# Optimization experiments

Measured on AMD Instinct MI355X. Metric: run time of the kernel, lower is better.

The kernel has to match this reference:

```python
import jax, jax.numpy as jnp
import numpy as np

B, N, D, H = 2, 2048, 1024, 16
DH = D // H
DF = 4 * D
SCALE = D ** (-0.5)  # standard_scale=False -> dim**-0.5
EPS = 1e-5


def _ln(x, w, b):
    mu = jnp.mean(x, axis=-1, keepdims=True)
    var = jnp.mean(jnp.square(x - mu), axis=-1, keepdims=True)
    return (x - mu) * jax.lax.rsqrt(var + EPS) * w + b


def setup_inputs() -> dict:
    key = jax.random.key(0)
    ks = jax.random.split(key, 12)
    s = lambda fan_in: (1.0 / np.sqrt(fan_in))
    return {
        "x": jax.random.normal(ks[0], (B, N, D), jnp.float32),
        "gamma": jax.random.uniform(ks[1], (B, H), jnp.float32),
        "dist_matrix": jax.random.uniform(ks[2], (N, N), jnp.float32),
        "ln1_w": jnp.ones((D,), jnp.float32),
        "ln1_b": jnp.zeros((D,), jnp.float32),
        "qkv_w": jax.random.normal(ks[3], (D, 3 * D), jnp.float32) * s(D),
        "qkv_b": jnp.zeros((3 * D,), jnp.float32),
        "proj_w": jax.random.normal(ks[4], (D, D), jnp.float32) * s(D),
        "proj_b": jnp.zeros((D,), jnp.float32),
        "ln2_w": jnp.ones((D,), jnp.float32),
        "ln2_b": jnp.zeros((D,), jnp.float32),
        "mlp_w1": jax.random.normal(ks[5], (D, DF), jnp.float32) * s(D),
        "mlp_b1": jnp.zeros((DF,), jnp.float32),
        "mlp_w2": jax.random.normal(ks[6], (DF, D), jnp.float32) * s(DF),
        "mlp_b2": jnp.zeros((D,), jnp.float32),
    }


def reference(x, gamma, dist_matrix, ln1_w, ln1_b, qkv_w, qkv_b, proj_w, proj_b,
              ln2_w, ln2_b, mlp_w1, mlp_b1, mlp_w2, mlp_b2):
    # --- ZoomAttention on norm1(x) ---
    h = _ln(x, ln1_w, ln1_b)                                   # [B,N,D]
    qkv = h @ qkv_w + qkv_b                                    # [B,N,3D]
    qkv = qkv.reshape(B, N, 3, H, DH).transpose(2, 0, 3, 1, 4)  # [3,B,H,N,DH]
    q, k, v = qkv[0], qkv[1], qkv[2]
    scores = jnp.einsum("bhnd,bhmd->bhnm", q, k) * SCALE       # [B,H,N,N]
    scores = scores - gamma[:, :, None, None] * dist_matrix[None, None]
    attn = jax.nn.softmax(scores, axis=-1)
    out = jnp.einsum("bhnm,bhmd->bhnd", attn, v)               # [B,H,N,DH]
    out = out.transpose(0, 2, 1, 3).reshape(B, N, D)
    x = x + (out @ proj_w + proj_b)
    # --- MLP (exact GELU, torch default) ---
    h2 = _ln(x, ln2_w, ln2_b)
    h2 = jax.nn.gelu(h2 @ mlp_w1 + mlp_b1, approximate=False) @ mlp_w2 + mlp_b2
    return x + h2
```

## Files before the change

### kernel.cpp

```cpp
#include <hip/hip_runtime.h>
#include <hip/hip_bf16.h>


#define SCALE_ 0.03125f
#define EPS_   1e-5f
#define LOG2E_ 1.4426950408889634f
#define SC2_   (SCALE_ * LOG2E_)

typedef unsigned short u16;
typedef __attribute__((ext_vector_type(8))) short short8;
typedef __attribute__((ext_vector_type(4))) float f32x4;
typedef __attribute__((ext_vector_type(4))) unsigned short u16x4;

__device__ inline float b2f(u16 u){ unsigned x = ((unsigned)u) << 16; float f; __builtin_memcpy(&f, &x, 4); return f; }
__device__ inline u16 f2b(float f){ __hip_bfloat16 h = __float2bfloat16(f); u16 u; __builtin_memcpy(&u, &h, 2); return u; }

__device__ inline void glds16(const u16* g, u16* l) {
    __builtin_amdgcn_global_load_lds(
        (const __attribute__((address_space(1))) void*)g,
        (__attribute__((address_space(3))) void*)l, 16, 0, 0);
}

__global__ __launch_bounds__(256) void transpose_cast(const float* __restrict__ src,
                                                      u16* __restrict__ dst, int K, int N) {
    __shared__ float t[32][33];
    int nb = blockIdx.x * 32, kb = blockIdx.y * 32;
    int tx = threadIdx.x & 31, ty = threadIdx.x >> 5;
    for (int i = 0; i < 4; i++) {
        int r = ty + i * 8;
        t[r][tx] = src[(size_t)(kb + r) * N + nb + tx];
    }
    __syncthreads();
    for (int i = 0; i < 4; i++) {
        int r = ty + i * 8;
        dst[(size_t)(nb + r) * K + kb + tx] = f2b(t[tx][r]);
    }
}

__global__ __launch_bounds__(256) void cast_scale_bf16(const float* __restrict__ src,
                                                       u16* __restrict__ dst, int n4, float scale) {
    int i = blockIdx.x * 256 + threadIdx.x;
    if (i < n4) {
        float4 v = ((const float4*)src)[i];
        u16x4 o;
        o[0] = f2b(v.x * scale); o[1] = f2b(v.y * scale);
        o[2] = f2b(v.z * scale); o[3] = f2b(v.w * scale);
        ((u16x4*)dst)[i] = o;
    }
}

__global__ __launch_bounds__(256) void ln_bf16(const float* __restrict__ x,
                                               const float* __restrict__ w,
                                               const float* __restrict__ b,
                                               u16* __restrict__ out) {
    int row = blockIdx.x, t = threadIdx.x;
    float4 v = ((const float4*)(x + (size_t)row * 1024))[t];
    float s1 = v.x + v.y + v.z + v.w;
    float s2 = v.x * v.x + v.y * v.y + v.z * v.z + v.w * v.w;
    for (int o = 32; o > 0; o >>= 1) { s1 += __shfl_xor(s1, o); s2 += __shfl_xor(s2, o); }
    __shared__ float a1[4], a2[4];
    if ((t & 63) == 0) { a1[t >> 6] = s1; a2[t >> 6] = s2; }
    __syncthreads();
    s1 = a1[0] + a1[1] + a1[2] + a1[3];
    s2 = a2[0] + a2[1] + a2[2] + a2[3];
    float mu = s1 * (1.0f / 1024.0f);
    float var = s2 * (1.0f / 1024.0f) - mu * mu;
    float rs = rsqrtf(var + EPS_);
    float4 wv = ((const float4*)w)[t];
    float4 bv = ((const float4*)b)[t];
    u16x4 o;
    o[0] = f2b((v.x - mu) * rs * wv.x + bv.x);
    o[1] = f2b((v.y - mu) * rs * wv.y + bv.y);
    o[2] = f2b((v.z - mu) * rs * wv.z + bv.z);
    o[3] = f2b((v.w - mu) * rs * wv.w + bv.w);
    ((u16x4*)(out + (size_t)row * 1024))[t] = o;
}

template <int MODE, int BN>
__global__ __launch_bounds__(256) void gemm_bf16(
    const u16* __restrict__ A, const u16* __restrict__ Bt,
    const float* __restrict__ bias, int M, int N, int K,
    const float* __restrict__ res, float* __restrict__ outf, u16* __restrict__ outb,
    u16* __restrict__ qp, u16* __restrict__ kp, u16* __restrict__ vtp) {
    constexpr int NN = BN / 32;
    __shared__ u16 As[128 * 64];
    __shared__ u16 Bs[BN * 64];
    int br = blockIdx.y * 128, bc = blockIdx.x * BN;
    int tid = threadIdx.x;
    int w = tid >> 6, lane = tid & 63, g = lane >> 4, ln = lane & 15;
    int wr = (w >> 1) * 64, wc = (w & 1) * (BN / 2);
    f32x4 acc[4][NN] = {};
    int sgcol = (((lane & 7) ^ (lane >> 3)) << 3);
    int arow = w * 32 + (lane >> 3);
    int brow = w * (BN / 4) + (lane >> 3);
    const u16* Ap = A + (size_t)(br + arow) * K + sgcol;
    const u16* Bp = Bt + (size_t)(bc + brow) * K + sgcol;
    u16* lA = &As[(w * 32) * 64];
    u16* lB = &Bs[(w * (BN / 4)) * 64];
    size_t rstep = (size_t)8 * K;
    for (int kt = 0; kt < K; kt += 64) {
        __syncthreads();
        #pragma unroll
        for (int i = 0; i < 4; i++) glds16(Ap + kt + i * rstep, lA + i * 512);
        #pragma unroll
        for (int i = 0; i < BN / 32; i++) glds16(Bp + kt + i * rstep, lB + i * 512);
        __syncthreads();
        #pragma unroll
        for (int kk = 0; kk < 2; kk++) {
            int so = (((kk << 2) + g) ^ (ln & 7)) << 3;
            short8 af[4], bfr[NN];
            #pragma unroll
            for (int m = 0; m < 4; m++)  af[m]  = *(const short8*)&As[(wr + m * 16 + ln) * 64 + so];
            #pragma unroll
            for (int n = 0; n < NN; n++) bfr[n] = *(const short8*)&Bs[(wc + n * 16 + ln) * 64 + so];
            #pragma unroll
            for (int m = 0; m < 4; m++)
                #pragma unroll
                for (int n = 0; n < NN; n++)
                    acc[m][n] = __builtin_amdgcn_mfma_f32_16x16x32_bf16(af[m], bfr[n], acc[m][n], 0, 0, 0);
        }
    }
    #pragma unroll
    for (int m = 0; m < 4; m++) {
        int row0 = br + wr + m * 16 + g * 4;
        #pragma unroll
        for (int n = 0; n < NN; n++) {
            int col = bc + wc + n * 16 + ln;
            float bv = bias[col];
            if constexpr (MODE == 0) {
                int which = col >> 10, cc = col & 1023, hh = cc >> 6, dh = cc & 63;
                int bb = row0 >> 11, nn0 = row0 & 2047;
                size_t bh = (size_t)(bb * 16 + hh);
                if (which == 0) {
                    for (int r = 0; r < 4; r++)
                        qp[((bh * 2048 + nn0 + r) << 6) + dh] = f2b((acc[m][n][r] + bv) * SC2_);
                } else if (which == 1) {
                    for (int r = 0; r < 4; r++)
                        kp[((bh * 2048 + nn0 + r) << 6) + dh] = f2b(acc[m][n][r] + bv);
                } else {
                    u16x4 o;
                    for (int r = 0; r < 4; r++) o[r] = f2b(acc[m][n][r] + bv);
                    *(u16x4*)&vtp[((bh * 64 + dh) << 11) + nn0] = o;
                }
            } else if constexpr (MODE == 1) {
                for (int r = 0; r < 4; r++) {
                    size_t idx = (size_t)(row0 + r) * 1024 + col;
                    outf[idx] = res[idx] + acc[m][n][r] + bv;
                }
            } else if constexpr (MODE == 2) {
                for (int r = 0; r < 4; r++) {
                    float v = acc[m][n][r] + bv;
                    float gl = 0.5f * v * (1.0f + erff(v * 0.7071067811865476f));
                    outb[(size_t)(row0 + r) * 4096 + col] = f2b(gl);
                }
            } else {
                for (int r = 0; r < 4; r++) {
                    size_t idx = (size_t)(row0 + r) * 1024 + col;
                    outf[idx] = outf[idx] + acc[m][n][r] + bv;
                }
            }
        }
    }
}

__global__ __launch_bounds__(256) void attn_fwd(
    const u16* __restrict__ qg, const u16* __restrict__ kg, const u16* __restrict__ vtg,
    const u16* __restrict__ distb, const float* __restrict__ gamma, u16* __restrict__ ao) {
    __shared__ u16 Ks[2][64 * 64];
    __shared__ u16 Vs[2][64 * 64];
    __shared__ u16 Ps[4][16 * 64];
    int qt = blockIdx.x, bh = blockIdx.y;
    int b = bh >> 4, h = bh & 15;
    int tid = threadIdx.x, w = tid >> 6, lane = tid & 63, g = lane >> 4, ln = lane & 15;
    float gam = gamma[bh];
    int qglob = qt * 64 + w * 16 + ln;
    const u16* qrow = qg + ((size_t)bh * 2048 + qglob) * 64;
    short8 qf0 = *(const short8*)(qrow + g * 8);
    short8 qf1 = *(const short8*)(qrow + 32 + g * 8);
    const u16* dbase = distb + (size_t)qglob * 2048 + g * 4;
    float m2 = -3.0e38f, lsum = 0.0f;
    f32x4 acco[4] = {};
    int srow = tid >> 2, sc = (tid & 3) * 2;
    int ss0 = ((sc ^ (srow & 7)) << 3), ss1 = (((sc + 1) ^ (srow & 7)) << 3);
    const u16* kgp = kg + ((size_t)bh * 2048 + srow) * 64 + sc * 8;
    const u16* vgp = vtg + ((size_t)bh * 64 + srow) * 2048 + sc * 8;
    {
        short8 a0 = *(const short8*)(kgp);
        short8 a1 = *(const short8*)(kgp + 8);
        short8 c0 = *(const short8*)(vgp);
        short8 c1 = *(const short8*)(vgp + 8);
        *(short8*)&Ks[0][srow * 64 + ss0] = a0;
        *(short8*)&Ks[0][srow * 64 + ss1] = a1;
        *(short8*)&Vs[0][srow * 64 + ss0] = c0;
        *(short8*)&Vs[0][srow * 64 + ss1] = c1;
    }
    u16x4 dcv[4];
    #pragma unroll
    for (int nb = 0; nb < 4; nb++) dcv[nb] = *(const u16x4*)(dbase + nb * 16);
    __syncthreads();
    int cur = 0;
    int so0 = (g ^ (ln & 7)) << 3, so1 = ((4 + g) ^ (ln & 7)) << 3;
    for (int kt = 0; kt < 32; kt++) {
        short8 kr0, kr1, vr0, vr1;
        u16x4 dnx[4];
        if (kt < 31) {
            kr0 = *(const short8*)(kgp + (kt + 1) * 4096);
            kr1 = *(const short8*)(kgp + (kt + 1) * 4096 + 8);
            vr0 = *(const short8*)(vgp + (kt + 1) * 64);
            vr1 = *(const short8*)(vgp + (kt + 1) * 64 + 8);
            #pragma unroll
            for (int nb = 0; nb < 4; nb++)
                dnx[nb] = *(const u16x4*)(dbase + (kt + 1) * 64 + nb * 16);
        }
        f32x4 sa[4] = {};
        __builtin_amdgcn_s_setprio(1);
        #pragma unroll
        for (int nb = 0; nb < 4; nb++) {
            short8 kf0 = *(const short8*)&Ks[cur][(nb * 16 + ln) * 64 + so0];
            short8 kf1 = *(const short8*)&Ks[cur][(nb * 16 + ln) * 64 + so1];
            sa[nb] = __builtin_amdgcn_mfma_f32_16x16x32_bf16(kf0, qf0, sa[nb], 0, 0, 0);
            sa[nb] = __builtin_amdgcn_mfma_f32_16x16x32_bf16(kf1, qf1, sa[nb], 0, 0, 0);
        }
        __builtin_amdgcn_s_setprio(0);
        float sv[4][4], pm = -3.0e38f;
        #pragma unroll
        for (int nb = 0; nb < 4; nb++)
            #pragma unroll
            for (int r = 0; r < 4; r++) {
                float s = sa[nb][r] - gam * b2f(dcv[nb][r]);
                sv[nb][r] = s;
                pm = fmaxf(pm, s);
            }
        pm = fmaxf(pm, __shfl_xor(pm, 16));
        pm = fmaxf(pm, __shfl_xor(pm, 32));
        if (!__all(pm - m2 <= 8.0f)) {
            float nm = fmaxf(m2, pm);
            float al = __builtin_exp2f(m2 - nm);
            m2 = nm;
            lsum *= al;
            #pragma unroll
            for (int db = 0; db < 4; db++) acco[db] *= al;
        }
        float ps = 0.0f;
        #pragma unroll
        for (int nb = 0; nb < 4; nb++) {
            u16x4 pw;
            #pragma unroll
            for (int r = 0; r < 4; r++) {
                float p = __builtin_exp2f(sv[nb][r] - m2);
                ps += p;
                pw[r] = f2b(p);
            }
            int off = nb * 16 + g * 4;
            *(u16x4*)&Ps[w][ln * 64 + (((off >> 3) ^ (ln & 7)) << 3) + (off & 7)] = pw;
        }
        ps += __shfl_xor(ps, 16);
        ps += __shfl_xor(ps, 32);
        lsum += ps;
        short8 pf0 = *(const short8*)&Ps[w][ln * 64 + so0];
        short8 pf1 = *(const short8*)&Ps[w][ln * 64 + so1];
        __builtin_amdgcn_s_setprio(1);
        #pragma unroll
        for (int db = 0; db < 4; db++) {
            short8 vf0 = *(const short8*)&Vs[cur][(db * 16 + ln) * 64 + so0];
            short8 vf1 = *(const short8*)&Vs[cur][(db * 16 + ln) * 64 + so1];
            acco[db] = __builtin_amdgcn_mfma_f32_16x16x32_bf16(vf0, pf0, acco[db], 0, 0, 0);
            acco[db] = __builtin_amdgcn_mfma_f32_16x16x32_bf16(vf1, pf1, acco[db], 0, 0, 0);
        }
        __builtin_amdgcn_s_setprio(0);
        if (kt < 31) {
            int nx = cur ^ 1;
            *(short8*)&Ks[nx][srow * 64 + ss0] = kr0;
            *(short8*)&Ks[nx][srow * 64 + ss1] = kr1;
            *(short8*)&Vs[nx][srow * 64 + ss0] = vr0;
            *(short8*)&Vs[nx][srow * 64 + ss1] = vr1;
            #pragma unroll
            for (int nb = 0; nb < 4; nb++) dcv[nb] = dnx[nb];
            __syncthreads();
            cur = nx;
        }
    }
    float inv = 1.0f / lsum;
    u16* aop = ao + (size_t)(b * 2048 + qglob) * 1024 + h * 64 + g * 4;
    #pragma unroll
    for (int db = 0; db < 4; db++) {
        u16x4 o;
        #pragma unroll
        for (int r = 0; r < 4; r++) o[r] = f2b(acco[db][r] * inv);
        *(u16x4*)(aop + db * 16) = o;
    }
}

extern "C" void kernel_launch(void* const* d_in, const int* in_sizes, int n_in,
                              void* d_out, int out_size, void* d_ws, size_t ws_size,
                              hipStream_t stream) {
    const float* x     = (const float*)d_in[0];
    const float* gamma = (const float*)d_in[1];
    const float* dist  = (const float*)d_in[2];
    const float* ln1w  = (const float*)d_in[3];
    const float* ln1b  = (const float*)d_in[4];
    const float* qkvw  = (const float*)d_in[5];
    const float* qkvb  = (const float*)d_in[6];
    const float* projw = (const float*)d_in[7];
    const float* projb = (const float*)d_in[8];
    const float* ln2w  = (const float*)d_in[9];
    const float* ln2b  = (const float*)d_in[10];
    const float* w1    = (const float*)d_in[11];
    const float* b1    = (const float*)d_in[12];
    const float* w2    = (const float*)d_in[13];
    const float* b2    = (const float*)d_in[14];
    float* out = (float*)d_out;
    char* ws = (char*)d_ws;
    u16* wqkvT  = (u16*)(ws + 0);
    u16* wprojT = (u16*)(ws + 6291456);
    u16* w1T    = (u16*)(ws + 8388608);
    u16* w2T    = (u16*)(ws + 16777216);
    u16* distb  = (u16*)(ws + 25165824);
    u16* hb     = (u16*)(ws + 33554432);
    u16* qb     = (u16*)(ws + 41943040);
    u16* kb     = (u16*)(ws + 50331648);
    u16* vtb    = (u16*)(ws + 58720256);
    u16* aob    = (u16*)(ws + 67108864);
    u16* gb     = hb;
    u16* h2b    = aob;

    dim3 blk(256);
    transpose_cast<<<dim3(3072 / 32, 1024 / 32), blk, 0, stream>>>(qkvw, wqkvT, 1024, 3072);
    transpose_cast<<<dim3(1024 / 32, 1024 / 32), blk, 0, stream>>>(projw, wprojT, 1024, 1024);
    transpose_cast<<<dim3(4096 / 32, 1024 / 32), blk, 0, stream>>>(w1, w1T, 1024, 4096);
    transpose_cast<<<dim3(1024 / 32, 4096 / 32), blk, 0, stream>>>(w2, w2T, 4096, 1024);
    cast_scale_bf16<<<4096, blk, 0, stream>>>(dist, distb, 2048 * 2048 / 4, LOG2E_);
    ln_bf16<<<4096, blk, 0, stream>>>(x, ln1w, ln1b, hb);
    gemm_bf16<0, 128><<<dim3(24, 32), blk, 0, stream>>>(hb, wqkvT, qkvb, 4096, 3072, 1024,
                                                        nullptr, nullptr, nullptr, qb, kb, vtb);
    attn_fwd<<<dim3(32, 32), blk, 0, stream>>>(qb, kb, vtb, distb, gamma, aob);
    gemm_bf16<1, 64><<<dim3(16, 32), blk, 0, stream>>>(aob, wprojT, projb, 4096, 1024, 1024,
                                                       x, out, nullptr, nullptr, nullptr, nullptr);
    ln_bf16<<<4096, blk, 0, stream>>>(out, ln2w, ln2b, h2b);
    gemm_bf16<2, 128><<<dim3(32, 32), blk, 0, stream>>>(h2b, w1T, b1, 4096, 4096, 1024,
                                                        nullptr, nullptr, gb, nullptr, nullptr, nullptr);
    gemm_bf16<3, 64><<<dim3(16, 32), blk, 0, stream>>>(gb, w2T, b2, 4096, 1024, 4096,
                                                       nullptr, out, nullptr, nullptr, nullptr, nullptr);
}
```

Measured before the change: 297.8 us.

## Add 256x256 pipelined GEMM, read fp32 dist directly, compute row sums via MFMA

```diff
diff --git a/kernel.cpp b/kernel.cpp
--- a/kernel.cpp
+++ b/kernel.cpp
@@ -34,18 +34,6 @@
     for (int i = 0; i < 4; i++) {
         int r = ty + i * 8;
         dst[(size_t)(nb + r) * K + kb + tx] = f2b(t[tx][r]);
-    }
-}
-
-__global__ __launch_bounds__(256) void cast_scale_bf16(const float* __restrict__ src,
-                                                       u16* __restrict__ dst, int n4, float scale) {
-    int i = blockIdx.x * 256 + threadIdx.x;
-    if (i < n4) {
-        float4 v = ((const float4*)src)[i];
-        u16x4 o;
-        o[0] = f2b(v.x * scale); o[1] = f2b(v.y * scale);
-        o[2] = f2b(v.z * scale); o[3] = f2b(v.w * scale);
-        ((u16x4*)dst)[i] = o;
     }
 }
 
@@ -76,12 +64,128 @@
     ((u16x4*)(out + (size_t)row * 1024))[t] = o;
 }
 
+template <int MODE>
+__global__ __launch_bounds__(512) void gemm256_8ph(
+    const u16* __restrict__ A, const u16* __restrict__ Bt,
+    const float* __restrict__ bias, int K,
+    u16* __restrict__ outb,
+    u16* __restrict__ qp, u16* __restrict__ kp, u16* __restrict__ vtp) {
+    __shared__ u16 LS[4][2][256 * 32];
+    int tid = threadIdx.x;
+    int w = tid >> 6, lane = tid & 63, g = lane >> 4, ln = lane & 15;
+    int wr = w >> 2, wc = w & 3;
+    int gx = gridDim.x;
+    int nwg = gx * gridDim.y;
+    int lin = blockIdx.y * gx + blockIdx.x;
+    int swz = (lin & 7) * (nwg >> 3) + (lin >> 3);
+    int bx = swz % gx, by = swz / gx;
+    int br = by * 256, bc = bx * 256;
+    int jx = (((lane & 3) ^ ((lane >> 3) & 3)) << 3);
+    const u16* Ast = A + (size_t)(br + w * 32 + (lane >> 2)) * K + jx;
+    const u16* Bst = Bt + (size_t)(bc + w * 32 + (lane >> 2)) * K + jx;
+    size_t r16 = (size_t)16 * K;
+    const int ldsW = (w * 32) * 32;
+    f32x4 acc[8][4] = {};
+    int NT = K >> 5;
+    int slotr = ((g ^ ((ln >> 1) & 3)) << 3);
+    for (int kt = 0; kt < 3; ++kt) {
+        glds16(Ast + (size_t)kt * 32, &LS[kt][0][ldsW]);
+        glds16(Ast + (size_t)kt * 32 + r16, &LS[kt][0][ldsW + 512]);
+        glds16(Bst + (size_t)kt * 32, &LS[kt][1][ldsW]);
+        glds16(Bst + (size_t)kt * 32 + r16, &LS[kt][1][ldsW + 512]);
+    }
+    asm volatile("s_waitcnt vmcnt(8)" ::: "memory");
+    __builtin_amdgcn_s_barrier();
+    short8 aa[4], bb[4];
+    for (int kt = 0; kt < NT; ++kt) {
+        const u16* bufA = &LS[kt & 3][0][0];
+        const u16* bufB = &LS[kt & 3][1][0];
+        int s3 = kt + 3;
+        #pragma unroll
+        for (int m = 0; m < 4; ++m)
+            aa[m] = *(const short8*)&bufA[(wr * 128 + m * 16 + ln) * 32 + slotr];
+        #pragma unroll
+        for (int n = 0; n < 4; ++n)
+            bb[n] = *(const short8*)&bufB[(wc * 64 + n * 16 + ln) * 32 + slotr];
+        if (s3 < NT) {
+            u16* d = &LS[s3 & 3][0][ldsW];
+            glds16(Ast + (size_t)s3 * 32, d);
+            glds16(Ast + (size_t)s3 * 32 + r16, d + 512);
+        }
+        __builtin_amdgcn_s_barrier();
+        asm volatile("s_waitcnt lgkmcnt(0)" ::: "memory");
+        __builtin_amdgcn_sched_barrier(0);
+        __builtin_amdgcn_s_setprio(1);
+        #pragma unroll
+        for (int m = 0; m < 4; ++m)
+            #pragma unroll
+            for (int n = 0; n < 4; ++n)
+                acc[m][n] = __builtin_amdgcn_mfma_f32_16x16x32_bf16(aa[m], bb[n], acc[m][n], 0, 0, 0);
+        __builtin_amdgcn_s_setprio(0);
+        __builtin_amdgcn_sched_barrier(0);
+        __builtin_amdgcn_s_barrier();
+        #pragma unroll
+        for (int m = 0; m < 4; ++m)
+            aa[m] = *(const short8*)&bufA[(wr * 128 + 64 + m * 16 + ln) * 32 + slotr];
+        if (s3 < NT) {
+            u16* d = &LS[s3 & 3][1][ldsW];
+            glds16(Bst + (size_t)s3 * 32, d);
+            glds16(Bst + (size_t)s3 * 32 + r16, d + 512);
+        }
+        if (kt + 3 < NT)      asm volatile("s_waitcnt vmcnt(8)" ::: "memory");
+        else if (kt + 2 < NT) asm volatile("s_waitcnt vmcnt(4)" ::: "memory");
+        else if (kt + 1 < NT) asm volatile("s_waitcnt vmcnt(0)" ::: "memory");
+        __builtin_amdgcn_s_barrier();
+        asm volatile("s_waitcnt lgkmcnt(0)" ::: "memory");
+        __builtin_amdgcn_sched_barrier(0);
+        __builtin_amdgcn_s_setprio(1);
+        #pragma unroll
+        for (int m = 0; m < 4; ++m)
+            #pragma unroll
+            for (int n = 0; n < 4; ++n)
+                acc[4 + m][n] = __builtin_amdgcn_mfma_f32_16x16x32_bf16(aa[m], bb[n], acc[4 + m][n], 0, 0, 0);
+        __builtin_amdgcn_s_setprio(0);
+        __builtin_amdgcn_sched_barrier(0);
+        __builtin_amdgcn_s_barrier();
+    }
+    #pragma unroll
+    for (int m = 0; m < 8; ++m) {
+        int row0 = br + wr * 128 + m * 16 + g * 4;
+        #pragma unroll
+        for (int n = 0; n < 4; ++n) {
+            int col = bc + wc * 64 + n * 16 + ln;
+            float bv = bias[col];
+            if constexpr (MODE == 0) {
+                int which = col >> 10, cc = col & 1023, hh = cc >> 6, dh = cc & 63;
+                int bb2 = row0 >> 11, nn0 = row0 & 2047;
+                size_t bh = (size_t)(bb2 * 16 + hh);
+                if (which == 0) {
+                    for (int r = 0; r < 4; r++)
+                        qp[((bh * 2048 + nn0 + r) << 6) + dh] = f2b((acc[m][n][r] + bv) * SC2_);
+                } else if (which == 1) {
+                    for (int r = 0; r < 4; r++)
+                        kp[((bh * 2048 + nn0 + r) << 6) + dh] = f2b(acc[m][n][r] + bv);
+                } else {
+                    u16x4 o;
+                    for (int r = 0; r < 4; r++) o[r] = f2b(acc[m][n][r] + bv);
+                    *(u16x4*)&vtp[((bh * 64 + dh) << 11) + nn0] = o;
+                }
+            } else {
+                for (int r = 0; r < 4; r++) {
+                    float v = acc[m][n][r] + bv;
+                    float gl = 0.5f * v * (1.0f + erff(v * 0.7071067811865476f));
+                    outb[(size_t)(row0 + r) * 4096 + col] = f2b(gl);
+                }
+            }
+        }
+    }
+}
+
 template <int MODE, int BN>
 __global__ __launch_bounds__(256) void gemm_bf16(
     const u16* __restrict__ A, const u16* __restrict__ Bt,
     const float* __restrict__ bias, int M, int N, int K,
-    const float* __restrict__ res, float* __restrict__ outf, u16* __restrict__ outb,
-    u16* __restrict__ qp, u16* __restrict__ kp, u16* __restrict__ vtp) {
+    const float* __restrict__ res, float* __restrict__ outf) {
     constexpr int NN = BN / 32;
     __shared__ u16 As[128 * 64];
     __shared__ u16 Bs[BN * 64];
@@ -127,31 +231,10 @@
         for (int n = 0; n < NN; n++) {
             int col = bc + wc + n * 16 + ln;
             float bv = bias[col];
-            if constexpr (MODE == 0) {
-                int which = col >> 10, cc = col & 1023, hh = cc >> 6, dh = cc & 63;
-                int bb = row0 >> 11, nn0 = row0 & 2047;
-                size_t bh = (size_t)(bb * 16 + hh);
-                if (which == 0) {
-                    for (int r = 0; r < 4; r++)
-                        qp[((bh * 2048 + nn0 + r) << 6) + dh] = f2b((acc[m][n][r] + bv) * SC2_);
-                } else if (which == 1) {
-                    for (int r = 0; r < 4; r++)
-                        kp[((bh * 2048 + nn0 + r) << 6) + dh] = f2b(acc[m][n][r] + bv);
-                } else {
-                    u16x4 o;
-                    for (int r = 0; r < 4; r++) o[r] = f2b(acc[m][n][r] + bv);
-                    *(u16x4*)&vtp[((bh * 64 + dh) << 11) + nn0] = o;
-                }
-            } else if constexpr (MODE == 1) {
+            if constexpr (MODE == 1) {
                 for (int r = 0; r < 4; r++) {
                     size_t idx = (size_t)(row0 + r) * 1024 + col;
                     outf[idx] = res[idx] + acc[m][n][r] + bv;
-                }
-            } else if constexpr (MODE == 2) {
-                for (int r = 0; r < 4; r++) {
-                    float v = acc[m][n][r] + bv;
-                    float gl = 0.5f * v * (1.0f + erff(v * 0.7071067811865476f));
-                    outb[(size_t)(row0 + r) * 4096 + col] = f2b(gl);
                 }
             } else {
                 for (int r = 0; r < 4; r++) {
@@ -165,21 +248,25 @@
 
 __global__ __launch_bounds__(256) void attn_fwd(
     const u16* __restrict__ qg, const u16* __restrict__ kg, const u16* __restrict__ vtg,
-    const u16* __restrict__ distb, const float* __restrict__ gamma, u16* __restrict__ ao) {
+    const float* __restrict__ dist, const float* __restrict__ gamma, u16* __restrict__ ao) {
     __shared__ u16 Ks[2][64 * 64];
     __shared__ u16 Vs[2][64 * 64];
     __shared__ u16 Ps[4][16 * 64];
     int qt = blockIdx.x, bh = blockIdx.y;
     int b = bh >> 4, h = bh & 15;
     int tid = threadIdx.x, w = tid >> 6, lane = tid & 63, g = lane >> 4, ln = lane & 15;
-    float gam = gamma[bh];
+    float gam2 = gamma[bh] * LOG2E_;
     int qglob = qt * 64 + w * 16 + ln;
     const u16* qrow = qg + ((size_t)bh * 2048 + qglob) * 64;
     short8 qf0 = *(const short8*)(qrow + g * 8);
     short8 qf1 = *(const short8*)(qrow + 32 + g * 8);
-    const u16* dbase = distb + (size_t)qglob * 2048 + g * 4;
-    float m2 = -3.0e38f, lsum = 0.0f;
+    const float* dbase = dist + (size_t)qglob * 2048 + g * 4;
+    float m2 = -3.0e38f;
     f32x4 acco[4] = {};
+    f32x4 accl = {};
+    short8 ones;
+    #pragma unroll
+    for (int i = 0; i < 8; ++i) ones[i] = (short)0x3F80;
     int srow = tid >> 2, sc = (tid & 3) * 2;
     int ss0 = ((sc ^ (srow & 7)) << 3), ss1 = (((sc + 1) ^ (srow & 7)) << 3);
     const u16* kgp = kg + ((size_t)bh * 2048 + srow) * 64 + sc * 8;
@@ -194,15 +281,15 @@
         *(short8*)&Vs[0][srow * 64 + ss0] = c0;
         *(short8*)&Vs[0][srow * 64 + ss1] = c1;
     }
-    u16x4 dcv[4];
+    float4 dcv[4];
     #pragma unroll
-    for (int nb = 0; nb < 4; nb++) dcv[nb] = *(const u16x4*)(dbase + nb * 16);
+    for (int nb = 0; nb < 4; nb++) dcv[nb] = *(const float4*)(dbase + nb * 16);
     __syncthreads();
     int cur = 0;
     int so0 = (g ^ (ln & 7)) << 3, so1 = ((4 + g) ^ (ln & 7)) << 3;
     for (int kt = 0; kt < 32; kt++) {
         short8 kr0, kr1, vr0, vr1;
-        u16x4 dnx[4];
+        float4 dnx[4];
         if (kt < 31) {
             kr0 = *(const short8*)(kgp + (kt + 1) * 4096);
             kr1 = *(const short8*)(kgp + (kt + 1) * 4096 + 8);
@@ -210,7 +297,7 @@
             vr1 = *(const short8*)(vgp + (kt + 1) * 64 + 8);
             #pragma unroll
             for (int nb = 0; nb < 4; nb++)
-                dnx[nb] = *(const u16x4*)(dbase + (kt + 1) * 64 + nb * 16);
+                dnx[nb] = *(const float4*)(dbase + (kt + 1) * 64 + nb * 16);
         }
         f32x4 sa[4] = {};
         __builtin_amdgcn_s_setprio(1);
@@ -224,39 +311,33 @@
         __builtin_amdgcn_s_setprio(0);
         float sv[4][4], pm = -3.0e38f;
         #pragma unroll
-        for (int nb = 0; nb < 4; nb++)
-            #pragma unroll
-            for (int r = 0; r < 4; r++) {
-                float s = sa[nb][r] - gam * b2f(dcv[nb][r]);
-                sv[nb][r] = s;
-                pm = fmaxf(pm, s);
-            }
+        for (int nb = 0; nb < 4; nb++) {
+            float4 dv = dcv[nb];
+            sv[nb][0] = sa[nb][0] - gam2 * dv.x;
+            sv[nb][1] = sa[nb][1] - gam2 * dv.y;
+            sv[nb][2] = sa[nb][2] - gam2 * dv.z;
+            sv[nb][3] = sa[nb][3] - gam2 * dv.w;
+            #pragma unroll
+            for (int r = 0; r < 4; r++) pm = fmaxf(pm, sv[nb][r]);
+        }
         pm = fmaxf(pm, __shfl_xor(pm, 16));
         pm = fmaxf(pm, __shfl_xor(pm, 32));
         if (!__all(pm - m2 <= 8.0f)) {
             float nm = fmaxf(m2, pm);
             float al = __builtin_exp2f(m2 - nm);
             m2 = nm;
-            lsum *= al;
+            accl *= al;
             #pragma unroll
             for (int db = 0; db < 4; db++) acco[db] *= al;
         }
-        float ps = 0.0f;
         #pragma unroll
         for (int nb = 0; nb < 4; nb++) {
             u16x4 pw;
             #pragma unroll
-            for (int r = 0; r < 4; r++) {
-                float p = __builtin_exp2f(sv[nb][r] - m2);
-                ps += p;
-                pw[r] = f2b(p);
-            }
+            for (int r = 0; r < 4; r++) pw[r] = f2b(__builtin_exp2f(sv[nb][r] - m2));
             int off = nb * 16 + g * 4;
             *(u16x4*)&Ps[w][ln * 64 + (((off >> 3) ^ (ln & 7)) << 3) + (off & 7)] = pw;
         }
-        ps += __shfl_xor(ps, 16);
-        ps += __shfl_xor(ps, 32);
-        lsum += ps;
         short8 pf0 = *(const short8*)&Ps[w][ln * 64 + so0];
         short8 pf1 = *(const short8*)&Ps[w][ln * 64 + so1];
         __builtin_amdgcn_s_setprio(1);
@@ -267,6 +348,8 @@
             acco[db] = __builtin_amdgcn_mfma_f32_16x16x32_bf16(vf0, pf0, acco[db], 0, 0, 0);
             acco[db] = __builtin_amdgcn_mfma_f32_16x16x32_bf16(vf1, pf1, acco[db], 0, 0, 0);
         }
+        accl = __builtin_amdgcn_mfma_f32_16x16x32_bf16(ones, pf0, accl, 0, 0, 0);
+        accl = __builtin_amdgcn_mfma_f32_16x16x32_bf16(ones, pf1, accl, 0, 0, 0);
         __builtin_amdgcn_s_setprio(0);
         if (kt < 31) {
             int nx = cur ^ 1;
@@ -280,7 +363,7 @@
             cur = nx;
         }
     }
-    float inv = 1.0f / lsum;
+    float inv = 1.0f / accl[0];
     u16* aop = ao + (size_t)(b * 2048 + qglob) * 1024 + h * 64 + g * 4;
     #pragma unroll
     for (int db = 0; db < 4; db++) {
@@ -315,7 +398,6 @@
     u16* wprojT = (u16*)(ws + 6291456);
     u16* w1T    = (u16*)(ws + 8388608);
     u16* w2T    = (u16*)(ws + 16777216);
-    u16* distb  = (u16*)(ws + 25165824);
     u16* hb     = (u16*)(ws + 33554432);
     u16* qb     = (u16*)(ws + 41943040);
     u16* kb     = (u16*)(ws + 50331648);
@@ -329,16 +411,15 @@
     transpose_cast<<<dim3(1024 / 32, 1024 / 32), blk, 0, stream>>>(projw, wprojT, 1024, 1024);
     transpose_cast<<<dim3(4096 / 32, 1024 / 32), blk, 0, stream>>>(w1, w1T, 1024, 4096);
     transpose_cast<<<dim3(1024 / 32, 4096 / 32), blk, 0, stream>>>(w2, w2T, 4096, 1024);
-    cast_scale_bf16<<<4096, blk, 0, stream>>>(dist, distb, 2048 * 2048 / 4, LOG2E_);
     ln_bf16<<<4096, blk, 0, stream>>>(x, ln1w, ln1b, hb);
-    gemm_bf16<0, 128><<<dim3(24, 32), blk, 0, stream>>>(hb, wqkvT, qkvb, 4096, 3072, 1024,
-                                                        nullptr, nullptr, nullptr, qb, kb, vtb);
-    attn_fwd<<<dim3(32, 32), blk, 0, stream>>>(qb, kb, vtb, distb, gamma, aob);
+    gemm256_8ph<0><<<dim3(12, 16), dim3(512), 0, stream>>>(hb, wqkvT, qkvb, 1024,
+                                                           nullptr, qb, kb, vtb);
+    attn_fwd<<<dim3(32, 32), blk, 0, stream>>>(qb, kb, vtb, dist, gamma, aob);
     gemm_bf16<1, 64><<<dim3(16, 32), blk, 0, stream>>>(aob, wprojT, projb, 4096, 1024, 1024,
-                                                       x, out, nullptr, nullptr, nullptr, nullptr);
+                                                       x, out);
     ln_bf16<<<4096, blk, 0, stream>>>(out, ln2w, ln2b, h2b);
-    gemm_bf16<2, 128><<<dim3(32, 32), blk, 0, stream>>>(h2b, w1T, b1, 4096, 4096, 1024,
-                                                        nullptr, nullptr, gb, nullptr, nullptr, nullptr);
+    gemm256_8ph<2><<<dim3(16, 16), dim3(512), 0, stream>>>(h2b, w1T, b1, 1024,
+                                                           gb, nullptr, nullptr, nullptr);
     gemm_bf16<3, 64><<<dim3(16, 32), blk, 0, stream>>>(gb, w2T, b2, 4096, 1024, 4096,
-                                                       nullptr, out, nullptr, nullptr, nullptr, nullptr);
-}
+                                                       nullptr, out);
+}
```

Result: no change. 297.2 us (-0.2%).
